# Kernel optimization log

Measured on AMD Instinct MI355X. Metric: run time of the kernel, lower is better.

Reference implementation:

```python
import jax, jax.numpy as jnp
import numpy as np

B, N, H = 512, 100, 768
I = 2 * H  # intermediate_dim default = hidden_dim * 2
NUM_ANS = 16
MAX_ANS = 15
LN_EPS = 1e-5


def setup_inputs() -> dict:
    key = jax.random.key(0)
    ks = jax.random.split(key, 7)
    s = 0.02
    return {
        "v_emb": jax.random.normal(ks[0], (B, N, H), dtype=jnp.float32),
        "W1": jax.random.normal(ks[1], (H, I), dtype=jnp.float32) * s,
        "b1": jax.random.normal(ks[2], (I,), dtype=jnp.float32) * s,
        "gamma": jnp.ones((I,), dtype=jnp.float32),
        "beta": jnp.zeros((I,), dtype=jnp.float32),
        "W2": jax.random.normal(ks[3], (I, 1), dtype=jnp.float32) * s,
        "b2": jax.random.normal(ks[4], (1,), dtype=jnp.float32) * s,
    }


def reference(v_emb, W1, b1, gamma, beta, W2, b2):
    # Linear -> GELU (exact/erf, torch nn.GELU default) -> LayerNorm -> Linear
    h = jnp.einsum("bnh,hi->bni", v_emb, W1) + b1            # [B,N,I]
    h = jax.nn.gelu(h, approximate=False)
    mu = jnp.mean(h, axis=-1, keepdims=True)
    var = jnp.mean(jnp.square(h - mu), axis=-1, keepdims=True)
    h = (h - mu) * jax.lax.rsqrt(var + LN_EPS) * gamma + beta
    scores = jnp.einsum("bni,io->bno", h, W2) + b2           # [B,N,1]
    scores = jax.nn.sigmoid(scores)                           # sigmoid=True branch
    pred = jnp.sum(scores, axis=1)                            # [B,1]
    # pred_to_logits: vectorized round + clamp + one-hot scatter
    # str(int(round(p))) in {'0'..'15'} -> that id; negative -> 0; overflow -> max_ans
    aid = jnp.clip(jnp.round(pred[:, 0]).astype(jnp.int32), 0, MAX_ANS)
    logits = jax.nn.one_hot(aid, NUM_ANS, dtype=scores.dtype)  # [B,16]
    # original returns dict: scores, final_attention_map (==scores), pred, logits
    return scores, pred, logits
```

## Files before the change

kernel.cpp:

```cpp
#include <hip/hip_runtime.h>
#include <hip/hip_bf16.h>
#include <cstdint>
#include <cstddef>

#define BB   512
#define NN   100
#define HH   768
#define II   1536
#define MM   (BB*NN)

typedef __bf16 bf16;
typedef __bf16 bf16x8 __attribute__((ext_vector_type(8)));
typedef float  f32x4  __attribute__((ext_vector_type(4)));

__device__ __forceinline__ void gld_lds16(const void* g, void* l) {
    __builtin_amdgcn_global_load_lds(
        (const __attribute__((address_space(1))) void*)g,
        (__attribute__((address_space(3))) void*)l, 16, 0, 0);
}

template <int CTRL>
__device__ __forceinline__ float ror_add(float x) {
    int y = __builtin_amdgcn_update_dpp(0, __float_as_int(x), CTRL, 0xF, 0xF, false);
    return x + __int_as_float(y);
}
__device__ __forceinline__ float red16(float x) {
    x = ror_add<0x121>(x);
    x = ror_add<0x122>(x);
    x = ror_add<0x124>(x);
    x = ror_add<0x128>(x);
    return x;
}

__device__ __forceinline__ float fast_gelu(float x) {
    const float ax = fabsf(x) * 0.70710678118654752f;
    const float t  = __builtin_amdgcn_rcpf(fmaf(0.3275911f, ax, 1.0f));
    float p = fmaf(1.061405429f, t, -1.453152027f);
    p = fmaf(p, t, 1.421413741f);
    p = fmaf(p, t, -0.284496736f);
    p = fmaf(p, t, 0.254829592f);
    p = p * t;
    const float e    = __expf(-ax * ax);
    const float erfa = fmaf(-p, e, 1.0f);
    const float erfx = copysignf(erfa, x);
    return 0.5f * x * (1.0f + erfx);
}

__global__ __launch_bounds__(256) void prep_w(
    const float* __restrict__ W1, const float* __restrict__ gamma,
    const float* __restrict__ beta, const float* __restrict__ W2,
    const float* __restrict__ b2,
    bf16* __restrict__ Wp, float* __restrict__ gw, float* __restrict__ scal)
{
    const int bid = blockIdx.x;
    if (bid < 576) {
        const int t = bid * 256 + threadIdx.x;
        const int n = t % II;
        const int g = t / II;
        const int p = (g & ~7) | ((g & 7) ^ (n & 7));
        bf16x8 o;
        #pragma unroll
        for (int i = 0; i < 8; ++i)
            o[i] = (bf16)W1[(size_t)(g * 8 + i) * II + n];
        *(bf16x8*)&Wp[(size_t)n * HH + p * 8] = o;
    } else if (bid == 576) {
        for (int j = threadIdx.x; j < II; j += 256)
            gw[j] = gamma[j] * W2[j];
    } else {
        float s1 = 0.f, s2 = 0.f;
        for (int j = threadIdx.x; j < II; j += 256) {
            float w2 = W2[j];
            s1 += gamma[j] * w2;
            s2 += beta[j]  * w2;
        }
        #pragma unroll
        for (int off = 32; off; off >>= 1) {
            s1 += __shfl_down(s1, off, 64);
            s2 += __shfl_down(s2, off, 64);
        }
        __shared__ float a1[4], a2[4];
        int lane = threadIdx.x & 63, w = threadIdx.x >> 6;
        if (lane == 0) { a1[w] = s1; a2[w] = s2; }
        __syncthreads();
        if (threadIdx.x == 0) {
            scal[0] = a1[0] + a1[1] + a1[2] + a1[3];
            scal[1] = a2[0] + a2[1] + a2[2] + a2[3] + b2[0];
        }
    }
}

__global__ __launch_bounds__(256) void gemm_part(
    const float* __restrict__ Af, const bf16* __restrict__ Wp,
    const float* __restrict__ b1, const float* __restrict__ gw,
    float* __restrict__ part)
{
    __shared__ float AsF[128 * 64];
    __shared__ bf16  Bs[128 * 64];
    __shared__ float sred[2][128][3];

    const int tid  = threadIdx.x;
    const int lin  = (blockIdx.x & 7) * 600 + (blockIdx.x >> 3);
    const int mb   = lin / 12;
    const int nb   = lin % 12;
    const int lane = tid & 63;
    const int w    = tid >> 6;
    const int wm   = w >> 1;
    const int wn   = w & 1;
    const int m15  = lane & 15;
    const int q    = lane >> 4;
    const int row0 = mb * 128;

    const int arow = tid >> 4;
    const int ac   = tid & 15;
    const int acs  = (ac & 8) | ((ac & 7) ^ (arow & 7));
    const float* aPf = Af + (size_t)(row0 + arow) * HH + acs * 4;
    float* asD = AsF + tid * 4;

    const int srow = tid >> 3;
    const int sc   = tid & 7;
    const bf16* bP = Wp + (size_t)(nb * 128 + srow) * HH + sc * 8;
    bf16* bsD = Bs + tid * 8;

    f32x4 acc[4][4] = {};

    for (int kt = 0; kt < 12; ++kt) {
        const float* ak = aPf + kt * 64;
        const bf16*  bk = bP  + kt * 64;
        #pragma unroll
        for (int i = 0; i < 8; ++i)
            gld_lds16(ak + (size_t)(16 * i) * HH, asD + i * 1024);
        #pragma unroll
        for (int i = 0; i < 4; ++i)
            gld_lds16(bk + (size_t)(32 * i) * HH, bsD + i * 2048);
        asm volatile("s_waitcnt vmcnt(0)" ::: "memory");
        __syncthreads();

        #pragma unroll
        for (int kb = 0; kb < 2; ++kb) {
            const int xb = ((kb * 4 + q) ^ (m15 & 7)) * 8;
            const int p0 = (2 * q) ^ (m15 & 7);
            bf16x8 af[4];
            #pragma unroll
            for (int mt = 0; mt < 4; ++mt) {
                const int r = wm*64 + mt*16 + m15;
                const f32x4* Arow = (const f32x4*)&AsF[r*64 + kb*32];
                f32x4 lo = Arow[p0];
                f32x4 hi = Arow[p0 ^ 1];
                af[mt] = (bf16x8){ (bf16)lo[0],(bf16)lo[1],(bf16)lo[2],(bf16)lo[3],
                                   (bf16)hi[0],(bf16)hi[1],(bf16)hi[2],(bf16)hi[3] };
            }
            #pragma unroll
            for (int nt = 0; nt < 4; ++nt) {
                bf16x8 bfr = *(const bf16x8*)&Bs[(wn*64 + nt*16 + m15)*64 + xb];
                #pragma unroll
                for (int mt = 0; mt < 4; ++mt)
                    acc[mt][nt] = __builtin_amdgcn_mfma_f32_16x16x32_bf16(
                        af[mt], bfr, acc[mt][nt], 0, 0, 0);
            }
        }
        __syncthreads();
    }

    float bv[4], gv[4];
    #pragma unroll
    for (int nt = 0; nt < 4; ++nt) {
        const int col = nb*128 + wn*64 + nt*16 + m15;
        bv[nt] = b1[col];
        gv[nt] = gw[col];
    }

    #pragma unroll
    for (int mt = 0; mt < 4; ++mt) {
        #pragma unroll
        for (int r = 0; r < 4; ++r) {
            float x0 = 0.f, x1 = 0.f, x2 = 0.f;
            #pragma unroll
            for (int nt = 0; nt < 4; ++nt) {
                float g = fast_gelu(acc[mt][nt][r] + bv[nt]);
                x0 += g; x1 += g * g; x2 += g * gv[nt];
            }
            x0 = red16(x0); x1 = red16(x1); x2 = red16(x2);
            if (m15 == 0) {
                const int rl = wm*64 + mt*16 + q*4 + r;
                sred[wn][rl][0] = x0;
                sred[wn][rl][1] = x1;
                sred[wn][rl][2] = x2;
            }
        }
    }
    __syncthreads();

    if (tid < 128) {
        const size_t rg = (size_t)row0 + tid;
        #pragma unroll
        for (int s = 0; s < 3; ++s)
            part[(size_t)s * 12 * MM + (size_t)nb * MM + rg]
                = sred[0][tid][s] + sred[1][tid][s];
    }
}

__global__ __launch_bounds__(128) void score_pred(
    const float* __restrict__ part, const float* __restrict__ scal,
    float* __restrict__ o_scores, float* __restrict__ o_pred,
    float* __restrict__ o_logits)
{
    const int b = blockIdx.x, t = threadIdx.x;
    float s = 0.f;
    if (t < NN) {
        const size_t row = (size_t)b * NN + t;
        float Sh = 0.f, Shh = 0.f, Shg = 0.f;
        #pragma unroll
        for (int j = 0; j < 12; ++j) {
            Sh  += part[(size_t)0*12*MM + (size_t)j*MM + row];
            Shh += part[(size_t)1*12*MM + (size_t)j*MM + row];
            Shg += part[(size_t)2*12*MM + (size_t)j*MM + row];
        }
        const float mu   = Sh * (1.0f / II);
        const float var  = Shh * (1.0f / II) - mu * mu;
        const float rstd = rsqrtf(var + 1e-5f);
        const float z    = rstd * (Shg - mu * scal[0]) + scal[1];
        s = 1.0f / (1.0f + __expf(-z));
        o_scores[row] = s;
    }
    float v = s;
    #pragma unroll
    for (int off = 32; off; off >>= 1) v += __shfl_down(v, off, 64);
    __shared__ float ssum[2];
    const int lane = t & 63, w = t >> 6;
    if (lane == 0) ssum[w] = v;
    __syncthreads();
    const float p = ssum[0] + ssum[1];
    if (t == 0) o_pred[b] = p;
    if (t < 16) {
        int aid = (int)rintf(p);
        aid = aid < 0 ? 0 : (aid > 15 ? 15 : aid);
        o_logits[b * 16 + t] = (t == aid) ? 1.0f : 0.0f;
    }
}

extern "C" void kernel_launch(void* const* d_in, const int* in_sizes, int n_in,
                              void* d_out, int out_size, void* d_ws, size_t ws_size,
                              hipStream_t stream)
{
    const float* v_emb = (const float*)d_in[0];
    const float* W1    = (const float*)d_in[1];
    const float* b1    = (const float*)d_in[2];
    const float* gamma = (const float*)d_in[3];
    const float* beta  = (const float*)d_in[4];
    const float* W2    = (const float*)d_in[5];
    const float* b2    = (const float*)d_in[6];

    char* ws = (char*)d_ws;
    size_t off = 0;
    bf16*  Wp   = (bf16*)(ws + off);  off += (size_t)II * HH * 2;
    float* gw   = (float*)(ws + off); off += (size_t)II * 4;
    float* scal = (float*)(ws + off); off += 256;
    float* part = (float*)(ws + off); off += (size_t)MM * 36 * 4;

    float* out       = (float*)d_out;
    float* o_scores  = out;
    float* o_pred    = out + MM;
    float* o_logits  = out + MM + BB;

    hipLaunchKernelGGL(prep_w, dim3(578), dim3(256), 0, stream,
                       W1, gamma, beta, W2, b2, Wp, gw, scal);
    hipLaunchKernelGGL(gemm_part, dim3((MM / 128) * 12), dim3(256),
                       0, stream, v_emb, Wp, b1, gw, part);
    hipLaunchKernelGGL(score_pred, dim3(BB), dim3(128), 0, stream,
                       part, scal, o_scores, o_pred, o_logits);
}
```

Baseline: 451.9 us.

## Prefetch A into registers, convert to bf16 once, double-buffer B in LDS

The GEMM main loop now loads the fp32 A tile for the next k-step into registers and stages the next B tile into a second LDS buffer via async global-to-LDS copies, while the current step's MFMAs run. A is converted to bf16 once when written to LDS, so the per-wave redundant fp32-to-bf16 conversion during fragment reads goes away and A's LDS footprint halves. The aim is to hide global-memory latency and cut conversion ALU work, at the cost of more registers and relying on hand-written vmcnt counts and raw s_barrier for correctness.

```diff
diff --git a/kernel.cpp b/kernel.cpp
--- a/kernel.cpp
+++ b/kernel.cpp
@@ -94,8 +94,8 @@
     const float* __restrict__ b1, const float* __restrict__ gw,
     float* __restrict__ part)
 {
-    __shared__ float AsF[128 * 64];
-    __shared__ bf16  Bs[128 * 64];
+    __shared__ bf16  As[8192];
+    __shared__ bf16  Bs[2 * 8192];
     __shared__ float sred[2][128][3];
 
     const int tid  = threadIdx.x;
@@ -110,56 +110,85 @@
     const int q    = lane >> 4;
     const int row0 = mb * 128;
 
-    const int arow = tid >> 4;
-    const int ac   = tid & 15;
-    const int acs  = (ac & 8) | ((ac & 7) ^ (arow & 7));
-    const float* aPf = Af + (size_t)(row0 + arow) * HH + acs * 4;
-    float* asD = AsF + tid * 4;
-
     const int srow = tid >> 3;
     const int sc   = tid & 7;
-    const bf16* bP = Wp + (size_t)(nb * 128 + srow) * HH + sc * 8;
-    bf16* bsD = Bs + tid * 8;
+    const int asel = sc ^ (srow & 7);
+    const float* aPf = Af + (size_t)(row0     + srow) * HH + asel * 8;
+    const bf16*  bP  = Wp + (size_t)(nb * 128 + srow) * HH + sc * 8;
+    bf16* asW = As + tid * 8;
+    bf16* bsW = Bs + tid * 8;
+
+    f32x4 av0[4], av1[4];
+
+#define LOADA(T) do {                                                       \
+    _Pragma("unroll")                                                       \
+    for (int i = 0; i < 4; ++i) {                                           \
+        const float* s = aPf + (size_t)(32 * i) * HH + (T) * 64;            \
+        av0[i] = *(const f32x4*)(s);                                        \
+        av1[i] = *(const f32x4*)(s + 4);                                    \
+    }                                                                       \
+} while (0)
+
+#define CVTWRITE() do {                                                     \
+    _Pragma("unroll")                                                       \
+    for (int i = 0; i < 4; ++i) {                                           \
+        bf16x8 o = { (bf16)av0[i][0],(bf16)av0[i][1],                       \
+                     (bf16)av0[i][2],(bf16)av0[i][3],                       \
+                     (bf16)av1[i][0],(bf16)av1[i][1],                       \
+                     (bf16)av1[i][2],(bf16)av1[i][3] };                     \
+        *(bf16x8*)(asW + i * 2048) = o;                                     \
+    }                                                                       \
+} while (0)
+
+#define STAGEB(T, BUF) do {                                                 \
+    const bf16* _b = bP + (T) * 64;                                         \
+    _Pragma("unroll")                                                       \
+    for (int i = 0; i < 4; ++i)                                             \
+        gld_lds16(_b + (size_t)(32 * i) * HH, bsW + (BUF) * 8192 + i * 2048);\
+} while (0)
 
     f32x4 acc[4][4] = {};
 
+    LOADA(0);
+    STAGEB(0, 0);
+
     for (int kt = 0; kt < 12; ++kt) {
-        const float* ak = aPf + kt * 64;
-        const bf16*  bk = bP  + kt * 64;
-        #pragma unroll
-        for (int i = 0; i < 8; ++i)
-            gld_lds16(ak + (size_t)(16 * i) * HH, asD + i * 1024);
-        #pragma unroll
-        for (int i = 0; i < 4; ++i)
-            gld_lds16(bk + (size_t)(32 * i) * HH, bsD + i * 2048);
-        asm volatile("s_waitcnt vmcnt(0)" ::: "memory");
-        __syncthreads();
+        const int buf = kt & 1;
+
+        CVTWRITE();
+
+        if (kt < 11) {
+            LOADA(kt + 1);
+            STAGEB(kt + 1, buf ^ 1);
+            asm volatile("s_waitcnt vmcnt(12) lgkmcnt(0)" ::: "memory");
+        } else {
+            asm volatile("s_waitcnt vmcnt(0) lgkmcnt(0)" ::: "memory");
+        }
+        __builtin_amdgcn_s_barrier();
 
         #pragma unroll
         for (int kb = 0; kb < 2; ++kb) {
-            const int xb = ((kb * 4 + q) ^ (m15 & 7)) * 8;
-            const int p0 = (2 * q) ^ (m15 & 7);
+            const int xsel = ((kb * 4 + q) ^ (m15 & 7)) * 8;
             bf16x8 af[4];
             #pragma unroll
-            for (int mt = 0; mt < 4; ++mt) {
-                const int r = wm*64 + mt*16 + m15;
-                const f32x4* Arow = (const f32x4*)&AsF[r*64 + kb*32];
-                f32x4 lo = Arow[p0];
-                f32x4 hi = Arow[p0 ^ 1];
-                af[mt] = (bf16x8){ (bf16)lo[0],(bf16)lo[1],(bf16)lo[2],(bf16)lo[3],
-                                   (bf16)hi[0],(bf16)hi[1],(bf16)hi[2],(bf16)hi[3] };
-            }
+            for (int mt = 0; mt < 4; ++mt)
+                af[mt] = *(const bf16x8*)&As[(wm*64 + mt*16 + m15)*64 + xsel];
             #pragma unroll
             for (int nt = 0; nt < 4; ++nt) {
-                bf16x8 bfr = *(const bf16x8*)&Bs[(wn*64 + nt*16 + m15)*64 + xb];
+                bf16x8 bfr = *(const bf16x8*)
+                    &Bs[buf*8192 + (wn*64 + nt*16 + m15)*64 + xsel];
                 #pragma unroll
                 for (int mt = 0; mt < 4; ++mt)
                     acc[mt][nt] = __builtin_amdgcn_mfma_f32_16x16x32_bf16(
                         af[mt], bfr, acc[mt][nt], 0, 0, 0);
             }
         }
-        __syncthreads();
-    }
+        __builtin_amdgcn_s_barrier();
+    }
+
+#undef LOADA
+#undef CVTWRITE
+#undef STAGEB
 
     float bv[4], gv[4];
     #pragma unroll
```

After: 423.4 us. 6.3% less time.
